# Performance work log

Hardware: AMD Instinct MI355X
Metric: run time of the kernel (lower is better)

## Reference

```python
import jax, jax.numpy as jnp
import numpy as np

B, QL, D = 4, 1024, 1024
H, HD = 16, 64
KVL = 2048


def setup_inputs() -> dict:
    key = jax.random.key(0)
    ks = jax.random.split(key, 6)
    scale = 1.0 / np.sqrt(D)
    return {
        "hidden_states": jax.random.normal(ks[0], (B, QL, D), dtype=jnp.float32),
        "key_states": jax.random.normal(ks[1], (B, H, KVL, HD), dtype=jnp.float32),
        "value_states": jax.random.normal(ks[2], (B, H, KVL, HD), dtype=jnp.float32),
        "attention_mask": jnp.zeros((B, 1, 1, KVL), dtype=jnp.float32),
        "Wq": jax.random.normal(ks[3], (D, D), dtype=jnp.float32) * scale,
        "Wo": jax.random.normal(ks[4], (D, D), dtype=jnp.float32) * scale,
    }


def reference(hidden_states, key_states, value_states, attention_mask, Wq, Wo):
    batch = hidden_states.shape[0]
    # Q projection (T5 Linear has no bias), split heads: [B, H, Q, HD]
    q = jnp.einsum("bqd,de->bqe", hidden_states, Wq)
    q = q.reshape(batch, -1, H, HD).transpose(0, 2, 1, 3)
    # NOTE: T5 attention has NO 1/sqrt(d) scaling
    scores = jnp.einsum("bhqd,bhkd->bhqk", q, key_states) + attention_mask
    attn = jax.nn.softmax(scores.astype(jnp.float32), axis=-1).astype(scores.dtype)
    out = jnp.einsum("bhqk,bhkd->bhqd", attn, value_states)
    out = out.transpose(0, 2, 1, 3).reshape(batch, -1, H * HD)
    return jnp.einsum("bqe,ed->bqd", out, Wo)
```

## Files before the change

### kernel.cpp

```cpp
#include <hip/hip_runtime.h>
#include <hip/hip_bf16.h>
#include <hip/hip_fp16.h>
#include <stdint.h>

typedef _Float16 f16;
typedef _Float16 f16x2 __attribute__((ext_vector_type(2)));
typedef _Float16 f16x4 __attribute__((ext_vector_type(4)));
typedef _Float16 f16x8 __attribute__((ext_vector_type(8)));
typedef float f32x4 __attribute__((ext_vector_type(4)));
typedef float f32x16 __attribute__((ext_vector_type(16)));
typedef uint32_t u32x4 __attribute__((ext_vector_type(4)));

#define B_ 4
#define QL_ 1024
#define D_ 1024
#define H_ 16
#define HD_ 64
#define KVL_ 2048
#define L2E 1.44269504088896f

__device__ __forceinline__ void g2lds16(const void* g, void* l) {
    __builtin_amdgcn_global_load_lds(
        (const __attribute__((address_space(1))) uint32_t*)g,
        (__attribute__((address_space(3))) uint32_t*)l,
        16, 0, 0);
}

union U8 { uint32_t u[4]; f16x8 v; };

__device__ __forceinline__ uint32_t pkrtz(float a, float b) {
    auto t = __builtin_amdgcn_cvt_pkrtz(a, b);
    return __builtin_bit_cast(uint32_t, t);
}

__global__ void prep_wq(const float* __restrict__ Wq, f16* __restrict__ Wq_t) {
    __shared__ float t[64][65];
    int b2 = blockIdx.x, tid = threadIdx.x;
    int k0 = (b2 >> 4) << 6, n0 = (b2 & 15) << 6;
    int rr = tid >> 4, c4 = (tid & 15) << 2;
#pragma unroll
    for (int i = 0; i < 4; ++i) {
        int r = i * 16 + rr;
        float4 v = *(const float4*)(Wq + (size_t)(k0 + r) * 1024 + n0 + c4);
        t[r][c4 + 0] = v.x; t[r][c4 + 1] = v.y; t[r][c4 + 2] = v.z; t[r][c4 + 3] = v.w;
    }
    __syncthreads();
#pragma unroll
    for (int i = 0; i < 4; ++i) {
        int n = i * 16 + rr;
        f16x4 o;
#pragma unroll
        for (int j = 0; j < 4; ++j) o[j] = (f16)t[c4 + j][n];
        *(f16x4*)(Wq_t + (size_t)(n0 + n) * 1024 + k0 + c4) = o;
    }
}

__global__ __launch_bounds__(512) void gemm0_fused(
    const float* __restrict__ hs, const f16* __restrict__ BT, f16* __restrict__ q_h,
    const float* __restrict__ K, f16* __restrict__ K_h,
    const float* __restrict__ V, f16* __restrict__ V_t,
    const float* __restrict__ Wo, f16* __restrict__ Wo_t,
    const float* __restrict__ mask, f16* __restrict__ em16) {
    __shared__ char shmem[49152];
    int bid = blockIdx.x, tid = threadIdx.x;

    if (bid < 512) {
        char* Alds = shmem;
        char* Blds = shmem + 32768;
        int xcd = bid & 7, sx = bid >> 3;
        int bm = xcd * 4 + (sx & 3);
        int bn = sx >> 2;
        int w = tid >> 6, l = tid & 63;
        int l15 = l & 15, lg = l >> 4;
        int wm = w >> 1, wn = w & 1;
        f32x4 acc[2][2] = {};

        int rA0 = tid >> 3, c80 = tid & 7, cc0 = c80 ^ (rA0 & 7);
        const float* ags0 = hs + ((size_t)(bm * 128 + rA0) * 1024 + cc0 * 8);
        const float* ags1 = ags0 + 65536;
        int aw0 = rA0 * 128 + c80 * 16;
        int aw1 = aw0 + 8192;

        int rB = w * 8 + (l >> 3);
        int ccB = (l & 7) ^ (rB & 7);
        const char* bgp = (const char*)BT + ((size_t)(bn * 64 + rB) * 1024 + ccB * 8) * 2;
        int boB = w * 1024;

        int aoff[2][2], boff[2][2];
#pragma unroll
        for (int ks = 0; ks < 2; ++ks)
#pragma unroll
            for (int m = 0; m < 2; ++m) {
                int ra = wm * 32 + m * 16 + l15;
                aoff[ks][m] = ra * 128 + ((ks * 64 + lg * 16) ^ ((ra & 7) << 4));
                int rb = wn * 32 + m * 16 + l15;
                boff[ks][m] = rb * 128 + ((ks * 64 + lg * 16) ^ ((rb & 7) << 4));
            }

        f32x4 a0, a1, a2, a3;
#define ALOAD(buf, o32, oB)                                    \
    {                                                          \
        a0 = *(const f32x4*)(ags0 + (o32));                    \
        a1 = *(const f32x4*)(ags0 + (o32) + 4);                \
        a2 = *(const f32x4*)(ags1 + (o32));                    \
        a3 = *(const f32x4*)(ags1 + (o32) + 4);                \
        g2lds16(bgp + (oB), Blds + (buf) * 8192 + boB);        \
    }
#define CVTW(buf)                                                              \
    {                                                                          \
        asm volatile("s_waitcnt vmcnt(1)" ::: "memory");                       \
        u32x4 w0 = { pkrtz(a0[0], a0[1]), pkrtz(a0[2], a0[3]),                 \
                     pkrtz(a1[0], a1[1]), pkrtz(a1[2], a1[3]) };               \
        *(u32x4*)(Alds + (buf) * 16384 + aw0) = w0;                            \
        u32x4 w1 = { pkrtz(a2[0], a2[1]), pkrtz(a2[2], a2[3]),                 \
                     pkrtz(a3[0], a3[1]), pkrtz(a3[2], a3[3]) };               \
        *(u32x4*)(Alds + (buf) * 16384 + aw1) = w1;                            \
    }
#define GCOMP(buf)                                                               \
    _Pragma("unroll") for (int ks = 0; ks < 2; ++ks) {                           \
        f16x8 af[2], bf[2];                                                      \
        af[0] = *(const f16x8*)(Alds + (buf) * 16384 + aoff[ks][0]);             \
        af[1] = *(const f16x8*)(Alds + (buf) * 16384 + aoff[ks][1]);             \
        bf[0] = *(const f16x8*)(Blds + (buf) * 8192 + boff[ks][0]);              \
        bf[1] = *(const f16x8*)(Blds + (buf) * 8192 + boff[ks][1]);              \
        _Pragma("unroll") for (int m = 0; m < 2; ++m)                            \
            _Pragma("unroll") for (int n = 0; n < 2; ++n)                        \
                acc[m][n] = __builtin_amdgcn_mfma_f32_16x16x32_f16(af[m], bf[n], acc[m][n], 0, 0, 0); \
    }
#define SYNCV()                                                          \
    {                                                                    \
        asm volatile("s_waitcnt vmcnt(0) lgkmcnt(0)" ::: "memory");      \
        __syncthreads();                                                 \
    }

        ALOAD(0, 0, 0);
        CVTW(0);
        SYNCV();
        for (int t2 = 0; t2 < 8; ++t2) {
            ALOAD(1, 64, 128);
            GCOMP(0);
            CVTW(1);
            SYNCV();
            if (t2 < 7) ALOAD(0, 128, 256);
            GCOMP(1);
            if (t2 < 7) CVTW(0);
            SYNCV();
            ags0 += 128; ags1 += 128; bgp += 256;
        }
#pragma unroll
        for (int m = 0; m < 2; ++m)
#pragma unroll
            for (int n = 0; n < 2; ++n)
#pragma unroll
                for (int i = 0; i < 4; ++i) {
                    int row = bm * 128 + wm * 32 + m * 16 + lg * 4 + i;
                    int col = bn * 64 + wn * 32 + n * 16 + l15;
                    float v = acc[m][n][i] * L2E;
                    int b = row >> 10, q = row & 1023, h = col >> 6, d = col & 63;
                    q_h[(((size_t)b * H_ + h) * QL_ + q) * HD_ + d] = (f16)v;
                }
#undef ALOAD
#undef CVTW
#undef GCOMP
#undef SYNCV
    } else if (bid < 1536) {
        int t0 = (bid - 512) * 512 + tid;
#pragma unroll
        for (int rep = 0; rep < 2; ++rep) {
            int U = t0 + rep * 524288;
            int bh = U >> 14, rem = U & 16383;
            int ch = rem >> 9, r2 = rem & 511;
            int dsl = r2 >> 7, r3 = r2 & 127;
            int kv = r3 >> 1, hi2 = r3 & 1;
            const float* sp = K + (((size_t)bh * KVL_ + ch * 64 + kv) * HD_ + dsl * 16 + hi2 * 8);
            f16x8 o;
#pragma unroll
            for (int j = 0; j < 8; ++j) o[j] = (f16)sp[j];
            *(f16x8*)(K_h + (size_t)U * 8) = o;
        }
    } else if (bid < 2560) {
        int sub = tid >> 8, st2 = tid & 255;
        int vb = (bid - 1536) * 2 + sub;
        int bh = vb >> 5, ch = vb & 31;
        int b = bh >> 4;
        float (*tt)[65] = (float(*)[65])(shmem + sub * 16640);
        float* emv = (float*)(shmem + 33280 + sub * 256);
        int rr = st2 >> 4, c4 = (st2 & 15) << 2;
#pragma unroll
        for (int i = 0; i < 4; ++i) {
            int r = i * 16 + rr;
            float4 v = *(const float4*)(V + ((size_t)bh * KVL_ + ch * 64 + r) * HD_ + c4);
            tt[r][c4 + 0] = v.x; tt[r][c4 + 1] = v.y; tt[r][c4 + 2] = v.z; tt[r][c4 + 3] = v.w;
        }
        if (st2 < 64)
            emv[st2] = __builtin_amdgcn_exp2f(mask[(size_t)b * KVL_ + ch * 64 + st2] * L2E);
        __syncthreads();
#pragma unroll
        for (int rep = 0; rep < 2; ++rep) {
            int u = st2 + rep * 256;
            int st = u >> 7, d = (u >> 1) & 63, hi2 = u & 1;
            f16x8 o;
#pragma unroll
            for (int j = 0; j < 8; ++j) {
                int kvl = st * 16 + (j & 3) + 8 * (j >> 2) + 4 * hi2;
                o[j] = (f16)(tt[kvl][d] * emv[kvl]);
            }
            *(f16x8*)(V_t + ((size_t)(bh * 32 + ch) * 512 + u) * 8) = o;
        }
        if (((bh & 15) == 0) && st2 < 64) {
            int kb = st2 >> 5, hi2v = (st2 >> 4) & 1, slot = st2 & 15;
            int kvv = kb * 32 + (slot & 3) + 8 * (slot >> 2) + 4 * hi2v;
            em16[(((size_t)b * 64 + ch * 2 + kb) * 2 + hi2v) * 16 + slot] = (f16)emv[kvv];
        }
    } else {
        int sub = tid >> 8, st2 = tid & 255;
        int b2 = (bid - 2560) * 2 + sub;
        float (*tt)[65] = (float(*)[65])(shmem + sub * 16640);
        int k0 = (b2 >> 4) << 6, n0 = (b2 & 15) << 6;
        int rr = st2 >> 4, c4 = (st2 & 15) << 2;
#pragma unroll
        for (int i = 0; i < 4; ++i) {
            int r = i * 16 + rr;
            float4 v = *(const float4*)(Wo + (size_t)(k0 + r) * 1024 + n0 + c4);
            tt[r][c4 + 0] = v.x; tt[r][c4 + 1] = v.y; tt[r][c4 + 2] = v.z; tt[r][c4 + 3] = v.w;
        }
        __syncthreads();
#pragma unroll
        for (int i = 0; i < 4; ++i) {
            int n = i * 16 + rr;
            f16x4 o;
#pragma unroll
            for (int j = 0; j < 4; ++j) o[j] = (f16)tt[c4 + j][n];
            *(f16x4*)(Wo_t + (size_t)(n0 + n) * 1024 + k0 + c4) = o;
        }
    }
}

__global__ __launch_bounds__(512) void gemm_tn1(
    const f16* __restrict__ A, const f16* __restrict__ BT, float* __restrict__ Cout) {
    __shared__ char Alds[2][16384];
    __shared__ char Blds[2][8192];
    int d0 = blockIdx.x;
    int xcd = d0 & 7, sx = d0 >> 3;
    int bm = xcd * 4 + (sx & 3);
    int bn = sx >> 2;
    int tid = threadIdx.x, w = tid >> 6, l = tid & 63;
    int l15 = l & 15, lg = l >> 4;
    int wm = w >> 1, wn = w & 1;
    f32x4 acc[2][2] = {};

    const char* ag0; const char* ag1; int ao0, ao1;
    {
        int i0 = w, i1 = w + 8;
        int r0 = i0 * 8 + (l >> 3), r1 = i1 * 8 + (l >> 3);
        int c0 = (l & 7) ^ (r0 & 7), c1 = (l & 7) ^ (r1 & 7);
        ag0 = (const char*)A + ((size_t)(bm * 128 + r0) * 1024 + c0 * 8) * 2;
        ag1 = (const char*)A + ((size_t)(bm * 128 + r1) * 1024 + c1 * 8) * 2;
        ao0 = i0 * 1024; ao1 = i1 * 1024;
    }
    int rB = w * 8 + (l >> 3);
    int ccB = (l & 7) ^ (rB & 7);
    const char* bgp = (const char*)BT + ((size_t)(bn * 64 + rB) * 1024 + ccB * 8) * 2;
    int boB = w * 1024;

    int aoff[2][2], boff[2][2];
#pragma unroll
    for (int ks = 0; ks < 2; ++ks)
#pragma unroll
        for (int m = 0; m < 2; ++m) {
            int ra = wm * 32 + m * 16 + l15;
            aoff[ks][m] = ra * 128 + ((ks * 64 + lg * 16) ^ ((ra & 7) << 4));
            int rb = wn * 32 + m * 16 + l15;
            boff[ks][m] = rb * 128 + ((ks * 64 + lg * 16) ^ ((rb & 7) << 4));
        }
    const char* Ab = &Alds[0][0];
    const char* Bb = &Blds[0][0];

#define GSTAGE(buf, soff)                                      \
    {                                                          \
        g2lds16(ag0 + (soff), &Alds[buf][ao0]);                \
        g2lds16(ag1 + (soff), &Alds[buf][ao1]);                \
        g2lds16(bgp + (soff), &Blds[buf][boB]);                \
    }
#define GCOMP(buf)                                                               \
    _Pragma("unroll") for (int ks = 0; ks < 2; ++ks) {                           \
        f16x8 af[2], bf[2];                                                      \
        af[0] = *(const f16x8*)(Ab + (buf) * 16384 + aoff[ks][0]);               \
        af[1] = *(const f16x8*)(Ab + (buf) * 16384 + aoff[ks][1]);               \
        bf[0] = *(const f16x8*)(Bb + (buf) * 8192 + boff[ks][0]);                \
        bf[1] = *(const f16x8*)(Bb + (buf) * 8192 + boff[ks][1]);                \
        _Pragma("unroll") for (int m = 0; m < 2; ++m)                            \
            _Pragma("unroll") for (int n = 0; n < 2; ++n)                        \
                acc[m][n] = __builtin_amdgcn_mfma_f32_16x16x32_f16(af[m], bf[n], acc[m][n], 0, 0, 0); \
    }

    GSTAGE(0, 0);
    asm volatile("s_waitcnt vmcnt(0)" ::: "memory");
    __syncthreads();
    for (int t2 = 0; t2 < 8; ++t2) {
        GSTAGE(1, 128);
        GCOMP(0);
        asm volatile("s_waitcnt vmcnt(0)" ::: "memory");
        __syncthreads();
        if (t2 < 7) GSTAGE(0, 256);
        GCOMP(1);
        asm volatile("s_waitcnt vmcnt(0)" ::: "memory");
        __syncthreads();
        ag0 += 256; ag1 += 256; bgp += 256;
    }
#pragma unroll
    for (int m = 0; m < 2; ++m)
#pragma unroll
        for (int n = 0; n < 2; ++n)
#pragma unroll
            for (int i = 0; i < 4; ++i) {
                int row = bm * 128 + wm * 32 + m * 16 + lg * 4 + i;
                int col = bn * 64 + wn * 32 + n * 16 + l15;
                Cout[(size_t)row * 1024 + col] = acc[m][n][i];
            }
#undef GSTAGE
#undef GCOMP
}

__global__ __launch_bounds__(256, 4) void attn_fused(
    const f16* __restrict__ qh, const f16* __restrict__ kh, const f16* __restrict__ vt,
    const f16* __restrict__ em16, f16* __restrict__ aout) {
    __shared__ char lds_buf[32768];
    __shared__ char em_lds[4096];
    __shared__ float frl[4][32];
    __shared__ float fr2[2][2][32];
    __shared__ float2 msx[2][32];

    int tid = threadIdx.x, w = tid >> 6, l = tid & 63;
    int l31 = l & 31, hi = l >> 5;
    int g = w >> 1, qsub = w & 1;
    int d0 = blockIdx.x;
    int xcd = d0 & 7, sx = d0 >> 3;
    int bh = xcd * 8 + (sx & 7);
    int qt = sx >> 3;
    int b = bh >> 4, h = bh & 15;

    const char* kread = lds_buf + g * 16384 + l31 * 32 + hi * 16;
    const char* vread = lds_buf + g * 16384 + 8192 + l31 * 32 + hi * 16;
    const char* embase = em_lds + hi * 32;

    f16x8 Qf[4];
    {
        const f16* qp = qh + ((size_t)bh * QL_ + qt * 64 + qsub * 32 + l31) * HD_ + hi * 8;
#pragma unroll
        for (int ds_ = 0; ds_ < 4; ++ds_) Qf[ds_] = *(const f16x8*)(qp + ds_ * 16);
    }

    const char* kgp = (const char*)kh + ((size_t)(bh * 32 + g * 16) * 512) * 16 + qsub * 4096 + l * 16;
    const char* vgp = (const char*)vt + ((size_t)(bh * 32 + g * 16) * 512) * 16 + qsub * 2048 + l * 16;
    char* klw = lds_buf + g * 16384 + qsub * 2048;
    char* vlw = lds_buf + g * 16384 + 8192 + qsub * 2048;

#define PREF(buf, ko, vo)                                      \
    {                                                          \
        g2lds16(kgp + (ko), klw + (buf) * 4096);               \
        g2lds16(kgp + (ko) + 2048, klw + (buf) * 4096 + 1024); \
        g2lds16(vgp + (vo), vlw + (buf) * 4096);               \
        g2lds16(vgp + (vo) + 1024, vlw + (buf) * 4096 + 1024); \
    }

    float mrun = -1e30f, ssA = 0.f, ssB = 0.f;
    f32x16 acc[2] = {};
    int emoff = g * 2048;

#define BODY(buf, emo)                                                                    \
    {                                                                                     \
        f32x16 St = {};                                                                   \
        __builtin_amdgcn_s_setprio(1);                                                    \
        _Pragma("unroll") for (int ds_ = 0; ds_ < 4; ++ds_) {                             \
            f16x8 kf = *(const f16x8*)(kread + (buf) * 4096 + ds_ * 1024);                \
            St = __builtin_amdgcn_mfma_f32_32x32x16_f16(kf, Qf[ds_], St, 0, 0, 0);        \
        }                                                                                 \
        __builtin_amdgcn_s_setprio(0);                                                    \
        float a0 = fmaxf(fmaxf(St[0], St[1]), St[2]);                                     \
        float a1 = fmaxf(fmaxf(St[3], St[4]), St[5]);                                     \
        float a2 = fmaxf(fmaxf(St[6], St[7]), St[8]);                                     \
        float a3 = fmaxf(fmaxf(St[9], St[10]), St[11]);                                   \
        float a4 = fmaxf(fmaxf(St[12], St[13]), St[14]);                                  \
        float lmax = fmaxf(fmaxf(fmaxf(a0, a1), St[15]), fmaxf(a2, fmaxf(a3, a4)));       \
        if (__any(lmax > mrun + 12.f)) {                                                  \
            float pm = fmaxf(lmax, __shfl_xor(lmax, 32));                                 \
            float mn = fmaxf(mrun, pm);                                                   \
            float fac = __builtin_amdgcn_exp2f(mrun - mn);                                \
            mrun = mn; ssA *= fac; ssB *= fac;                                            \
            frl[w][l31] = fac;                                                            \
            asm volatile("s_waitcnt lgkmcnt(0)" ::: "memory");                            \
            _Pragma("unroll") for (int g4 = 0; g4 < 4; ++g4) {                            \
                f32x4 fv = *(const f32x4*)&frl[w][g4 * 8 + hi * 4];                       \
                _Pragma("unroll") for (int c = 0; c < 2; ++c)                             \
                    _Pragma("unroll") for (int j = 0; j < 4; ++j)                         \
                        acc[c][g4 * 4 + j] *= fv[j];                                      \
            }                                                                             \
        }                                                                                 \
        uint32_t pk[8];                                                                   \
        _Pragma("unroll") for (int i = 0; i < 8; ++i) {                                   \
            float p0 = __builtin_amdgcn_exp2f(St[2 * i] - mrun);                          \
            float p1 = __builtin_amdgcn_exp2f(St[2 * i + 1] - mrun);                      \
            pk[i] = pkrtz(p0, p1);                                                        \
        }                                                                                 \
        U8 ea, eb;                                                                        \
        ea.v = *(const f16x8*)(embase + (emo));                                           \
        eb.v = *(const f16x8*)(embase + (emo) + 16);                                      \
        _Pragma("unroll") for (int i = 0; i < 4; ++i) {                                   \
            ssA = __builtin_amdgcn_fdot2(__builtin_bit_cast(f16x2, pk[2 * i]),            \
                                         __builtin_bit_cast(f16x2, (2 * i) < 4 ? ea.u[2 * i] : eb.u[2 * i - 4]), ssA, false); \
            ssB = __builtin_amdgcn_fdot2(__builtin_bit_cast(f16x2, pk[2 * i + 1]),        \
                                         __builtin_bit_cast(f16x2, (2 * i + 1) < 4 ? ea.u[2 * i + 1] : eb.u[2 * i - 3]), ssB, false); \
        }                                                                                 \
        __builtin_amdgcn_s_setprio(1);                                                    \
        _Pragma("unroll") for (int sti = 0; sti < 2; ++sti) {                             \
            U8 pa;                                                                        \
            pa.u[0] = pk[sti * 4 + 0]; pa.u[1] = pk[sti * 4 + 1];                         \
            pa.u[2] = pk[sti * 4 + 2]; pa.u[3] = pk[sti * 4 + 3];                         \
            _Pragma("unroll") for (int c = 0; c < 2; ++c) {                               \
                U8 vb;                                                                    \
                vb.v = *(const f16x8*)(vread + (buf) * 4096 + sti * 2048 + c * 1024);     \
                acc[c] = __builtin_amdgcn_mfma_f32_32x32x16_f16(pa.v, vb.v, acc[c], 0, 0, 0); \
            }                                                                             \
        }                                                                                 \
        __builtin_amdgcn_s_setprio(0);                                                    \
    }

    g2lds16((const char*)em16 + b * 4096 + w * 1024 + l * 16, em_lds + w * 1024);
    PREF(0, 0, 0);
    asm volatile("s_waitcnt vmcnt(0)" ::: "memory");
    __syncthreads();

    for (int it = 0; it < 16; ++it) {
        PREF(1, 1024, 4096);
        BODY(0, emoff);
        asm volatile("s_waitcnt vmcnt(0)" ::: "memory");
        __syncthreads();
        if (it < 15) PREF(0, 8192, 8192);
        BODY(1, emoff + 64);
        asm volatile("s_waitcnt vmcnt(0)" ::: "memory");
        __syncthreads();
        kgp += 8192; vgp += 8192; emoff += 128;
    }

    float ssum = ssA + ssB;
    ssum += __shfl_xor(ssum, 32);
    char* exch = lds_buf;
    if (g == 1) {
        int base = qsub * 8192 + l * 128;
#pragma unroll
        for (int i = 0; i < 8; ++i) {
            int c = i >> 2, j0 = (i & 3) * 4;
            f32x4 vv = { acc[c][j0], acc[c][j0 + 1], acc[c][j0 + 2], acc[c][j0 + 3] };
            *(f32x4*)(exch + base + ((i * 16) ^ ((l & 7) << 4))) = vv;
        }
        if (hi == 0) msx[qsub][l31] = make_float2(mrun, ssum);
    }
    __syncthreads();
    if (g == 0) {
        float2 mb = msx[qsub][l31];
        float m = fmaxf(mrun, mb.x);
        float fA = __builtin_amdgcn_exp2f(mrun - m);
        float fB = __builtin_amdgcn_exp2f(mb.x - m);
        float s = ssum * fA + mb.y * fB;
        float rinv = 1.0f / s;
        if (hi == 0) { fr2[qsub][0][l31] = fA * rinv; fr2[qsub][1][l31] = fB * rinv; }
        asm volatile("s_waitcnt lgkmcnt(0)" ::: "memory");
        int base = qsub * 8192 + l * 128;
#pragma unroll
        for (int c = 0; c < 2; ++c)
#pragma unroll
            for (int g4 = 0; g4 < 4; ++g4) {
                f32x4 gAv = *(const f32x4*)&fr2[qsub][0][g4 * 8 + hi * 4];
                f32x4 gBv = *(const f32x4*)&fr2[qsub][1][g4 * 8 + hi * 4];
                int i = c * 4 + g4;
                f32x4 pv = *(const f32x4*)(exch + base + ((i * 16) ^ ((l & 7) << 4)));
#pragma unroll
                for (int j = 0; j < 4; ++j) {
                    float o = acc[c][g4 * 4 + j] * gAv[j] + pv[j] * gBv[j];
                    int q = qt * 64 + qsub * 32 + g4 * 8 + hi * 4 + j;
                    int dd = c * 32 + l31;
                    aout[((size_t)b * QL_ + q) * D_ + h * HD_ + dd] = (f16)o;
                }
            }
    }
#undef PREF
#undef BODY
}

extern "C" void kernel_launch(void* const* d_in, const int* in_sizes, int n_in,
                              void* d_out, int out_size, void* d_ws, size_t ws_size,
                              hipStream_t stream) {
    const float* hs = (const float*)d_in[0];
    const float* K  = (const float*)d_in[1];
    const float* V  = (const float*)d_in[2];
    const float* mask = (const float*)d_in[3];
    const float* Wq = (const float*)d_in[4];
    const float* Wo = (const float*)d_in[5];
    float* out = (float*)d_out;
    char* ws = (char*)d_ws;

    f16* Wq_t = (f16*)(ws + 0);
    f16* Wo_t = (f16*)(ws + 2097152);
    f16* K_h  = (f16*)(ws + 4194304);
    f16* V_t  = (f16*)(ws + 20971520);
    f16* q_h  = (f16*)(ws + 37748736);
    f16* a_o  = (f16*)(ws + 46137344);
    f16* em16 = (f16*)(ws + 54525952);

    prep_wq<<<256, 256, 0, stream>>>(Wq, Wq_t);
    gemm0_fused<<<2688, 512, 0, stream>>>(hs, Wq_t, q_h, K, K_h, V, V_t,
                                          Wo, Wo_t, mask, em16);
    attn_fused<<<1024, 256, 0, stream>>>(q_h, K_h, V_t, em16, a_o);
    gemm_tn1<<<512, 512, 0, stream>>>(a_o, Wo_t, out);
}
```

Before: 107.3 us.

## Split attention KV across four waves per 32-query tile, dropping block barriers

Result: slower. 126.0 us (+17.4%).

```diff
diff --git a/kernel.cpp b/kernel.cpp
--- a/kernel.cpp
+++ b/kernel.cpp
@@ -322,58 +322,60 @@
 #undef GCOMP
 }
 
-__global__ __launch_bounds__(256, 4) void attn_fused(
+__global__ __launch_bounds__(256, 2) void attn_fused(
     const f16* __restrict__ qh, const f16* __restrict__ kh, const f16* __restrict__ vt,
     const f16* __restrict__ em16, f16* __restrict__ aout) {
-    __shared__ char lds_buf[32768];
+    __shared__ char lds_buf[65536];
     __shared__ char em_lds[4096];
     __shared__ float frl[4][32];
-    __shared__ float fr2[2][2][32];
-    __shared__ float2 msx[2][32];
+    __shared__ float fr4[4][32];
+    __shared__ float2 msx[3][32];
 
     int tid = threadIdx.x, w = tid >> 6, l = tid & 63;
     int l31 = l & 31, hi = l >> 5;
-    int g = w >> 1, qsub = w & 1;
     int d0 = blockIdx.x;
     int xcd = d0 & 7, sx = d0 >> 3;
     int bh = xcd * 8 + (sx & 7);
     int qt = sx >> 3;
     int b = bh >> 4, h = bh & 15;
 
-    const char* kread = lds_buf + g * 16384 + l31 * 32 + hi * 16;
-    const char* vread = lds_buf + g * 16384 + 8192 + l31 * 32 + hi * 16;
-    const char* embase = em_lds + hi * 32;
+    char* wbase = lds_buf + w * 16384;
+    const char* kread = wbase + l31 * 32 + hi * 16;
+    const char* vread = wbase + 4096 + l31 * 32 + hi * 16;
+    const char* embase = em_lds + w * 1024 + hi * 32;
 
     f16x8 Qf[4];
     {
-        const f16* qp = qh + ((size_t)bh * QL_ + qt * 64 + qsub * 32 + l31) * HD_ + hi * 8;
+        const f16* qp = qh + ((size_t)bh * QL_ + qt * 32 + l31) * HD_ + hi * 8;
 #pragma unroll
         for (int ds_ = 0; ds_ < 4; ++ds_) Qf[ds_] = *(const f16x8*)(qp + ds_ * 16);
     }
 
-    const char* kgp = (const char*)kh + ((size_t)(bh * 32 + g * 16) * 512) * 16 + qsub * 4096 + l * 16;
-    const char* vgp = (const char*)vt + ((size_t)(bh * 32 + g * 16) * 512) * 16 + qsub * 2048 + l * 16;
-    char* klw = lds_buf + g * 16384 + qsub * 2048;
-    char* vlw = lds_buf + g * 16384 + 8192 + qsub * 2048;
-
-#define PREF(buf, ko, vo)                                      \
-    {                                                          \
-        g2lds16(kgp + (ko), klw + (buf) * 4096);               \
-        g2lds16(kgp + (ko) + 2048, klw + (buf) * 4096 + 1024); \
-        g2lds16(vgp + (vo), vlw + (buf) * 4096);               \
-        g2lds16(vgp + (vo) + 1024, vlw + (buf) * 4096 + 1024); \
+    const char* kgp = (const char*)kh + (size_t)(bh * 32) * 8192 + (size_t)w * 65536 + l * 16;
+    const char* vgp = (const char*)vt + (size_t)(bh * 32) * 8192 + (size_t)w * 65536 + l * 16;
+
+#define PREF(buf, ko, vo)                                         \
+    {                                                             \
+        g2lds16(kgp + (ko), wbase + (buf) * 8192);                \
+        g2lds16(kgp + (ko) + 2048, wbase + (buf) * 8192 + 1024);  \
+        g2lds16(kgp + (ko) + 4096, wbase + (buf) * 8192 + 2048);  \
+        g2lds16(kgp + (ko) + 6144, wbase + (buf) * 8192 + 3072);  \
+        g2lds16(vgp + (vo), wbase + (buf) * 8192 + 4096);         \
+        g2lds16(vgp + (vo) + 1024, wbase + (buf) * 8192 + 5120);  \
+        g2lds16(vgp + (vo) + 2048, wbase + (buf) * 8192 + 6144);  \
+        g2lds16(vgp + (vo) + 3072, wbase + (buf) * 8192 + 7168);  \
     }
 
     float mrun = -1e30f, ssA = 0.f, ssB = 0.f;
     f32x16 acc[2] = {};
-    int emoff = g * 2048;
+    int emoff = 0;
 
 #define BODY(buf, emo)                                                                    \
     {                                                                                     \
         f32x16 St = {};                                                                   \
         __builtin_amdgcn_s_setprio(1);                                                    \
         _Pragma("unroll") for (int ds_ = 0; ds_ < 4; ++ds_) {                             \
-            f16x8 kf = *(const f16x8*)(kread + (buf) * 4096 + ds_ * 1024);                \
+            f16x8 kf = *(const f16x8*)(kread + (buf) * 8192 + ds_ * 1024);                \
             St = __builtin_amdgcn_mfma_f32_32x32x16_f16(kf, Qf[ds_], St, 0, 0, 0);        \
         }                                                                                 \
         __builtin_amdgcn_s_setprio(0);                                                    \
@@ -419,7 +421,7 @@
             pa.u[2] = pk[sti * 4 + 2]; pa.u[3] = pk[sti * 4 + 3];                         \
             _Pragma("unroll") for (int c = 0; c < 2; ++c) {                               \
                 U8 vb;                                                                    \
-                vb.v = *(const f16x8*)(vread + (buf) * 4096 + sti * 2048 + c * 1024);     \
+                vb.v = *(const f16x8*)(vread + (buf) * 8192 + sti * 2048 + c * 1024);     \
                 acc[c] = __builtin_amdgcn_mfma_f32_32x32x16_f16(pa.v, vb.v, acc[c], 0, 0, 0); \
             }                                                                             \
         }                                                                                 \
@@ -431,54 +433,64 @@
     asm volatile("s_waitcnt vmcnt(0)" ::: "memory");
     __syncthreads();
 
-    for (int it = 0; it < 16; ++it) {
+    for (int it = 0; it < 8; ++it) {
         PREF(1, 1024, 4096);
+        asm volatile("s_waitcnt vmcnt(8)" ::: "memory");
         BODY(0, emoff);
-        asm volatile("s_waitcnt vmcnt(0)" ::: "memory");
-        __syncthreads();
-        if (it < 15) PREF(0, 8192, 8192);
+        if (it < 7) PREF(0, 8192, 8192);
+        if (it < 7) { asm volatile("s_waitcnt vmcnt(8)" ::: "memory"); }
+        else        { asm volatile("s_waitcnt vmcnt(0)" ::: "memory"); }
         BODY(1, emoff + 64);
-        asm volatile("s_waitcnt vmcnt(0)" ::: "memory");
-        __syncthreads();
         kgp += 8192; vgp += 8192; emoff += 128;
     }
 
     float ssum = ssA + ssB;
     ssum += __shfl_xor(ssum, 32);
+    __syncthreads();
     char* exch = lds_buf;
-    if (g == 1) {
-        int base = qsub * 8192 + l * 128;
+    if (w > 0) {
+        int base = (w - 1) * 8192 + l * 128;
 #pragma unroll
         for (int i = 0; i < 8; ++i) {
             int c = i >> 2, j0 = (i & 3) * 4;
             f32x4 vv = { acc[c][j0], acc[c][j0 + 1], acc[c][j0 + 2], acc[c][j0 + 3] };
             *(f32x4*)(exch + base + ((i * 16) ^ ((l & 7) << 4))) = vv;
         }
-        if (hi == 0) msx[qsub][l31] = make_float2(mrun, ssum);
+        if (hi == 0) msx[w - 1][l31] = make_float2(mrun, ssum);
     }
     __syncthreads();
-    if (g == 0) {
-        float2 mb = msx[qsub][l31];
-        float m = fmaxf(mrun, mb.x);
-        float fA = __builtin_amdgcn_exp2f(mrun - m);
-        float fB = __builtin_amdgcn_exp2f(mb.x - m);
-        float s = ssum * fA + mb.y * fB;
+    if (w == 0) {
+        float2 m1 = msx[0][l31], m2 = msx[1][l31], m3 = msx[2][l31];
+        float m = fmaxf(fmaxf(mrun, m1.x), fmaxf(m2.x, m3.x));
+        float f0 = __builtin_amdgcn_exp2f(mrun - m);
+        float f1 = __builtin_amdgcn_exp2f(m1.x - m);
+        float f2 = __builtin_amdgcn_exp2f(m2.x - m);
+        float f3 = __builtin_amdgcn_exp2f(m3.x - m);
+        float s = f0 * ssum + f1 * m1.y + f2 * m2.y + f3 * m3.y;
         float rinv = 1.0f / s;
-        if (hi == 0) { fr2[qsub][0][l31] = fA * rinv; fr2[qsub][1][l31] = fB * rinv; }
+        if (hi == 0) {
+            fr4[0][l31] = f0 * rinv; fr4[1][l31] = f1 * rinv;
+            fr4[2][l31] = f2 * rinv; fr4[3][l31] = f3 * rinv;
+        }
         asm volatile("s_waitcnt lgkmcnt(0)" ::: "memory");
-        int base = qsub * 8192 + l * 128;
 #pragma unroll
         for (int c = 0; c < 2; ++c)
 #pragma unroll
             for (int g4 = 0; g4 < 4; ++g4) {
-                f32x4 gAv = *(const f32x4*)&fr2[qsub][0][g4 * 8 + hi * 4];
-                f32x4 gBv = *(const f32x4*)&fr2[qsub][1][g4 * 8 + hi * 4];
+                f32x4 w0v = *(const f32x4*)&fr4[0][g4 * 8 + hi * 4];
+                f32x4 w1v = *(const f32x4*)&fr4[1][g4 * 8 + hi * 4];
+                f32x4 w2v = *(const f32x4*)&fr4[2][g4 * 8 + hi * 4];
+                f32x4 w3v = *(const f32x4*)&fr4[3][g4 * 8 + hi * 4];
                 int i = c * 4 + g4;
-                f32x4 pv = *(const f32x4*)(exch + base + ((i * 16) ^ ((l & 7) << 4)));
+                int sw = (i * 16) ^ ((l & 7) << 4);
+                f32x4 p1 = *(const f32x4*)(exch + 0 * 8192 + l * 128 + sw);
+                f32x4 p2 = *(const f32x4*)(exch + 1 * 8192 + l * 128 + sw);
+                f32x4 p3 = *(const f32x4*)(exch + 2 * 8192 + l * 128 + sw);
 #pragma unroll
                 for (int j = 0; j < 4; ++j) {
-                    float o = acc[c][g4 * 4 + j] * gAv[j] + pv[j] * gBv[j];
-                    int q = qt * 64 + qsub * 32 + g4 * 8 + hi * 4 + j;
+                    float o = acc[c][g4 * 4 + j] * w0v[j] + p1[j] * w1v[j]
+                            + p2[j] * w2v[j] + p3[j] * w3v[j];
+                    int q = qt * 32 + g4 * 8 + hi * 4 + j;
                     int dd = c * 32 + l31;
                     aout[((size_t)b * QL_ + q) * D_ + h * HD_ + dd] = (f16)o;
                 }
@@ -511,6 +523,6 @@
     prep_wq<<<256, 256, 0, stream>>>(Wq, Wq_t);
     gemm0_fused<<<2688, 512, 0, stream>>>(hs, Wq_t, q_h, K, K_h, V, V_t,
                                           Wo, Wo_t, mask, em16);
-    attn_fused<<<1024, 256, 0, stream>>>(q_h, K_h, V_t, em16, a_o);
+    attn_fused<<<2048, 256, 0, stream>>>(q_h, K_h, V_t, em16, a_o);
     gemm_tn1<<<512, 512, 0, stream>>>(a_o, Wo_t, out);
 }
```

## Load K/V fragments directly from global into registers, dropping LDS staging and barriers

Applied to the files above, without the earlier changes.

Measured after the change: 108.9 us. No clear change (+1.4%).

```diff
diff --git a/kernel.cpp b/kernel.cpp
--- a/kernel.cpp
+++ b/kernel.cpp
@@ -322,10 +322,10 @@
 #undef GCOMP
 }
 
-__global__ __launch_bounds__(256, 4) void attn_fused(
+__global__ __launch_bounds__(256, 3) void attn_fused(
     const f16* __restrict__ qh, const f16* __restrict__ kh, const f16* __restrict__ vt,
     const f16* __restrict__ em16, f16* __restrict__ aout) {
-    __shared__ char lds_buf[32768];
+    __shared__ char exch[16384];
     __shared__ char em_lds[4096];
     __shared__ float frl[4][32];
     __shared__ float fr2[2][2][32];
@@ -340,8 +340,6 @@
     int qt = sx >> 3;
     int b = bh >> 4, h = bh & 15;
 
-    const char* kread = lds_buf + g * 16384 + l31 * 32 + hi * 16;
-    const char* vread = lds_buf + g * 16384 + 8192 + l31 * 32 + hi * 16;
     const char* embase = em_lds + hi * 32;
 
     f16x8 Qf[4];
@@ -351,31 +349,30 @@
         for (int ds_ = 0; ds_ < 4; ++ds_) Qf[ds_] = *(const f16x8*)(qp + ds_ * 16);
     }
 
-    const char* kgp = (const char*)kh + ((size_t)(bh * 32 + g * 16) * 512) * 16 + qsub * 4096 + l * 16;
-    const char* vgp = (const char*)vt + ((size_t)(bh * 32 + g * 16) * 512) * 16 + qsub * 2048 + l * 16;
-    char* klw = lds_buf + g * 16384 + qsub * 2048;
-    char* vlw = lds_buf + g * 16384 + 8192 + qsub * 2048;
-
-#define PREF(buf, ko, vo)                                      \
-    {                                                          \
-        g2lds16(kgp + (ko), klw + (buf) * 4096);               \
-        g2lds16(kgp + (ko) + 2048, klw + (buf) * 4096 + 1024); \
-        g2lds16(vgp + (vo), vlw + (buf) * 4096);               \
-        g2lds16(vgp + (vo) + 1024, vlw + (buf) * 4096 + 1024); \
+    const char* kgp = (const char*)kh + (size_t)(bh * 32 + g * 16) * 8192 + l31 * 32 + hi * 16;
+    const char* vgp = (const char*)vt + (size_t)(bh * 32 + g * 16) * 8192 + l31 * 32 + hi * 16;
+
+#define LOADK(dst, off)                                              \
+    {                                                                \
+        _Pragma("unroll") for (int i_ = 0; i_ < 4; ++i_)             \
+            dst[i_] = *(const f16x8*)(kgp + (off) + i_ * 2048);      \
+    }
+#define LOADV(dst, off)                                              \
+    {                                                                \
+        _Pragma("unroll") for (int i_ = 0; i_ < 4; ++i_)             \
+            dst[i_] = *(const f16x8*)(vgp + (off) + i_ * 1024);      \
     }
 
     float mrun = -1e30f, ssA = 0.f, ssB = 0.f;
     f32x16 acc[2] = {};
     int emoff = g * 2048;
 
-#define BODY(buf, emo)                                                                    \
+#define BODY(Kf, Vf, emo)                                                                 \
     {                                                                                     \
         f32x16 St = {};                                                                   \
         __builtin_amdgcn_s_setprio(1);                                                    \
-        _Pragma("unroll") for (int ds_ = 0; ds_ < 4; ++ds_) {                             \
-            f16x8 kf = *(const f16x8*)(kread + (buf) * 4096 + ds_ * 1024);                \
-            St = __builtin_amdgcn_mfma_f32_32x32x16_f16(kf, Qf[ds_], St, 0, 0, 0);        \
-        }                                                                                 \
+        _Pragma("unroll") for (int ds_ = 0; ds_ < 4; ++ds_)                               \
+            St = __builtin_amdgcn_mfma_f32_32x32x16_f16(Kf[ds_], Qf[ds_], St, 0, 0, 0);   \
         __builtin_amdgcn_s_setprio(0);                                                    \
         float a0 = fmaxf(fmaxf(St[0], St[1]), St[2]);                                     \
         float a1 = fmaxf(fmaxf(St[3], St[4]), St[5]);                                     \
@@ -417,35 +414,31 @@
             U8 pa;                                                                        \
             pa.u[0] = pk[sti * 4 + 0]; pa.u[1] = pk[sti * 4 + 1];                         \
             pa.u[2] = pk[sti * 4 + 2]; pa.u[3] = pk[sti * 4 + 3];                         \
-            _Pragma("unroll") for (int c = 0; c < 2; ++c) {                               \
-                U8 vb;                                                                    \
-                vb.v = *(const f16x8*)(vread + (buf) * 4096 + sti * 2048 + c * 1024);     \
-                acc[c] = __builtin_amdgcn_mfma_f32_32x32x16_f16(pa.v, vb.v, acc[c], 0, 0, 0); \
-            }                                                                             \
+            _Pragma("unroll") for (int c = 0; c < 2; ++c)                                 \
+                acc[c] = __builtin_amdgcn_mfma_f32_32x32x16_f16(pa.v, Vf[sti * 2 + c], acc[c], 0, 0, 0); \
         }                                                                                 \
         __builtin_amdgcn_s_setprio(0);                                                    \
     }
 
     g2lds16((const char*)em16 + b * 4096 + w * 1024 + l * 16, em_lds + w * 1024);
-    PREF(0, 0, 0);
+    f16x8 Ka[4], Kb[4], Va[4], Vb[4];
+    LOADK(Ka, 0);
     asm volatile("s_waitcnt vmcnt(0)" ::: "memory");
     __syncthreads();
 
     for (int it = 0; it < 16; ++it) {
-        PREF(1, 1024, 4096);
-        BODY(0, emoff);
-        asm volatile("s_waitcnt vmcnt(0)" ::: "memory");
-        __syncthreads();
-        if (it < 15) PREF(0, 8192, 8192);
-        BODY(1, emoff + 64);
-        asm volatile("s_waitcnt vmcnt(0)" ::: "memory");
-        __syncthreads();
+        LOADV(Va, 0);
+        LOADK(Kb, 1024);
+        BODY(Ka, Va, emoff);
+        LOADV(Vb, 4096);
+        if (it < 15) LOADK(Ka, 8192);
+        BODY(Kb, Vb, emoff + 64);
         kgp += 8192; vgp += 8192; emoff += 128;
     }
 
     float ssum = ssA + ssB;
     ssum += __shfl_xor(ssum, 32);
-    char* exch = lds_buf;
+    __syncthreads();
     if (g == 1) {
         int base = qsub * 8192 + l * 128;
 #pragma unroll
@@ -484,7 +477,8 @@
                 }
             }
     }
-#undef PREF
+#undef LOADK
+#undef LOADV
 #undef BODY
 }
 
```
